# Kernel tuning notes

Measured on AMD Instinct MI355X. Metric: run time of the kernel, lower is better.

Reference implementation:

```python
import jax, jax.numpy as jnp
import numpy as np

HID = 1024
NH = 16
HD = HID // NH  # 64
RANK = 16
B, L = 2, 2048


def setup_inputs() -> dict:
    key = jax.random.key(0)
    ks = jax.random.split(key, 9)
    s = 0.02
    return {
        "x": jax.random.normal(ks[0], (B, L, HID), dtype=jnp.float32),
        "Wq": jax.random.normal(ks[1], (HID, HID), dtype=jnp.float32) * s,
        "Wk": jax.random.normal(ks[2], (HID, HID), dtype=jnp.float32) * s,
        "Wv": jax.random.normal(ks[3], (HID, HID), dtype=jnp.float32) * s,
        "Wg": jax.random.normal(ks[4], (HID, HID), dtype=jnp.float32) * s,
        "Wgk1": jax.random.normal(ks[5], (HID, RANK), dtype=jnp.float32) * s,
        "Wgk2": jax.random.normal(ks[6], (RANK, HID), dtype=jnp.float32) * s,
        "bgk2": jnp.zeros((HID,), dtype=jnp.float32),
        "gamma": jnp.ones((HID,), dtype=jnp.float32),
        "beta": jnp.zeros((HID,), dtype=jnp.float32),
        "Wout": jax.random.normal(ks[7], (HID, HID), dtype=jnp.float32) * s,
    }


def reference(x, Wq, Wk, Wv, Wg, Wgk1, Wgk2, bgk2, gamma, beta, Wout):
    Bb, Ll, Hid = x.shape
    H, Dh = NH, HD
    # projections -> [B, L, H, Dh]
    q = (x @ Wq).reshape(Bb, Ll, H, Dh)
    k = (x @ Wk).reshape(Bb, Ll, H, Dh)
    v = (x @ Wv).reshape(Bb, Ll, H, Dh)
    gk = (jax.nn.log_sigmoid((x @ Wgk1) @ Wgk2 + bgk2) / 16.0).reshape(Bb, Ll, H, Dh)

    # time-major for scan: [L, B, H, Dh]
    qT = jnp.transpose(q, (1, 0, 2, 3))
    kT = jnp.transpose(k, (1, 0, 2, 3))
    vT = jnp.transpose(v, (1, 0, 2, 3))
    gT = jnp.transpose(gk, (1, 0, 2, 3))

    def step(state, inp):
        qt, kt, vt, gt = inp  # each [B, H, Dh]
        gate = jnp.exp(gt)
        # state[b,h,v_dim,k_dim]; gate applied along v_dim (matches torch code)
        state = state * gate[..., None] + vt[..., None] * kt[..., None, :]
        out_t = jnp.einsum('bhvk,bhk->bhv', state, qt)
        return state, out_t

    state0 = jnp.zeros((Bb, H, Dh, Dh), dtype=x.dtype)
    _, outs = jax.lax.scan(step, state0, (qT, kT, vT, gT))  # outs: [L, B, H, Dh]
    out = jnp.transpose(outs, (1, 0, 2, 3)).reshape(Bb, Ll, Hid)

    # LayerNorm over total_dim
    mu = out.mean(-1, keepdims=True)
    var = out.var(-1, keepdims=True)
    out = (out - mu) / jnp.sqrt(var + 1e-5) * gamma + beta

    # output gate + projection (dropout = identity in eval)
    out = out * jax.nn.silu(x @ Wg)
    return out @ Wout
```

## Files before the change

kernel.cpp:

```cpp
#include <hip/hip_runtime.h>
#include <cstdint>
#include <cstddef>

#define HIDS 1024
#define NHEAD 16
#define HDIM 64
#define LSEQ 2048
#define BBATCH 2
#define NROW (BBATCH * LSEQ)
#define CHUNK 64
#define NCHUNK (LSEQ / CHUNK)
#define RANK 16

typedef short short8 __attribute__((ext_vector_type(8)));
typedef float floatx4 __attribute__((ext_vector_type(4)));

__device__ __forceinline__ ushort f2bf(float f) {
  uint32_t u = __float_as_uint(f);
  uint32_t r = (u + 0x7fffu + ((u >> 16) & 1u)) >> 16;
  return (ushort)r;
}
__device__ __forceinline__ float bf2f(ushort u) {
  return __uint_as_float(((uint32_t)u) << 16);
}
__device__ __forceinline__ float logsig16(float z) {
  return (fminf(z, 0.f) - log1pf(expf(-fabsf(z)))) * (1.f / 16.f);
}

__device__ __forceinline__ void async_copy16(const void* g, void* l) {
  __builtin_amdgcn_global_load_lds(
      (const __attribute__((address_space(1))) void*)g,
      (__attribute__((address_space(3))) void*)l, 16, 0, 0);
}

__global__ __launch_bounds__(256) void cvt_x_kernel(const float* __restrict__ x,
                                                    ushort* __restrict__ xbf) {
  const int i = blockIdx.x * 256 + threadIdx.x;
  float4 f = *(const float4*)(x + (size_t)i * 4);
  ushort4 o;
  o.x = f2bf(f.x); o.y = f2bf(f.y); o.z = f2bf(f.z); o.w = f2bf(f.w);
  *(ushort4*)(xbf + (size_t)i * 4) = o;
}

__global__ __launch_bounds__(256) void transpose_w_kernel(
    const float* __restrict__ W0, const float* __restrict__ W1,
    const float* __restrict__ W2, const float* __restrict__ W3,
    const float* __restrict__ W4, ushort* __restrict__ T0,
    ushort* __restrict__ T1, ushort* __restrict__ T2, ushort* __restrict__ T3,
    ushort* __restrict__ T4) {
  const int z = blockIdx.z;
  const float* W = (z == 0) ? W0 : (z == 1) ? W1 : (z == 2) ? W2 : (z == 3) ? W3 : W4;
  ushort* T = (z == 0) ? T0 : (z == 1) ? T1 : (z == 2) ? T2 : (z == 3) ? T3 : T4;
  __shared__ float sl[64][65];
  const int tid = threadIdx.x;
  const int k0 = blockIdx.y * 64, n0 = blockIdx.x * 64;
  const int r = tid >> 2, c4 = (tid & 3) * 16;
#pragma unroll
  for (int i = 0; i < 4; ++i) {
    float4 f = *(const float4*)(W + (size_t)(k0 + r) * HIDS + n0 + c4 + i * 4);
    sl[r][c4 + i * 4 + 0] = f.x;
    sl[r][c4 + i * 4 + 1] = f.y;
    sl[r][c4 + i * 4 + 2] = f.z;
    sl[r][c4 + i * 4 + 3] = f.w;
  }
  __syncthreads();
  const int n = tid >> 2, kc = (tid & 3) * 16;
#pragma unroll
  for (int i = 0; i < 4; ++i) {
    int kk = kc + i * 4;
    ushort4 o;
    o.x = f2bf(sl[kk + 0][n]);
    o.y = f2bf(sl[kk + 1][n]);
    o.z = f2bf(sl[kk + 2][n]);
    o.w = f2bf(sl[kk + 3][n]);
    *(ushort4*)(T + (size_t)(n0 + n) * HIDS + k0 + kk) = o;
  }
}

__global__ __launch_bounds__(256) void weff_kernel(const float* __restrict__ Wgk1,
                                                   const float* __restrict__ Wgk2,
                                                   ushort* __restrict__ Wte) {
  __shared__ float sW1[64][17];
  __shared__ float sW2[16][65];
  const int tid = threadIdx.x;
  const int n0 = blockIdx.x * 64, k0 = blockIdx.y * 64;
  {
    const int kl = tid >> 2, r4 = (tid & 3) * 4;
    float4 f = *(const float4*)(Wgk1 + (size_t)(k0 + kl) * RANK + r4);
    sW1[kl][r4] = f.x; sW1[kl][r4 + 1] = f.y; sW1[kl][r4 + 2] = f.z; sW1[kl][r4 + 3] = f.w;
    const int rr = tid >> 4, nl = (tid & 15) * 4;
    float4 g = *(const float4*)(Wgk2 + (size_t)rr * HIDS + n0 + nl);
    sW2[rr][nl] = g.x; sW2[rr][nl + 1] = g.y; sW2[rr][nl + 2] = g.z; sW2[rr][nl + 3] = g.w;
  }
  __syncthreads();
  const int nl = tid & 63, kq = (tid >> 6) * 16;
  float w2[16];
#pragma unroll
  for (int r = 0; r < 16; ++r) w2[r] = sW2[r][nl];
  ushort ob[16];
#pragma unroll
  for (int i = 0; i < 16; ++i) {
    float s = 0.f;
#pragma unroll
    for (int r = 0; r < 16; ++r) s = fmaf(sW1[kq + i][r], w2[r], s);
    ob[i] = f2bf(s);
  }
#pragma unroll
  for (int i = 0; i < 2; ++i)
    *(short8*)(Wte + (size_t)(n0 + nl) * HIDS + k0 + kq + i * 8) = *(short8*)&ob[i * 8];
}

__global__ __launch_bounds__(256) void proj5_kernel(
    const ushort* __restrict__ xbf, const ushort* __restrict__ Wtq,
    const ushort* __restrict__ Wtk, const ushort* __restrict__ Wtv,
    const ushort* __restrict__ Wtg, const ushort* __restrict__ Wte,
    ushort* __restrict__ qb, ushort* __restrict__ kb, ushort* __restrict__ vb,
    ushort* __restrict__ gb, ushort* __restrict__ zb) {
  const int z = blockIdx.z;
  const ushort* Bt = (z == 0) ? Wtq : (z == 1) ? Wtk : (z == 2) ? Wtv
                     : (z == 3) ? Wtg : Wte;
  ushort* C = (z == 0) ? qb : (z == 1) ? kb : (z == 2) ? vb : (z == 3) ? gb : zb;
  __shared__ ushort As[2][128 * 32];
  __shared__ ushort Bs[2][128 * 32];
  const int tid = threadIdx.x;
  const int wave = tid >> 6, lane = tid & 63;
  const int wm = (wave >> 1) * 64, wn = (wave & 1) * 64;
  const int bm = blockIdx.y * 128, bn = blockIdx.x * 128;
  const int lrow = tid >> 2, lk8 = (tid & 3) * 8;
  const ushort* Ag = xbf + (size_t)(bm + lrow) * HIDS + lk8;
  const ushort* Bg = Bt + (size_t)(bn + lrow) * HIDS + lk8;
  char* A0 = (char*)&As[0][0] + tid * 16;
  char* A1 = (char*)&As[1][0] + tid * 16;
  char* B0 = (char*)&Bs[0][0] + tid * 16;
  char* B1 = (char*)&Bs[1][0] + tid * 16;

  floatx4 acc[4][4];
#pragma unroll
  for (int i = 0; i < 4; ++i)
#pragma unroll
    for (int j = 0; j < 4; ++j) acc[i][j] = (floatx4){0.f, 0.f, 0.f, 0.f};

  const int fm = lane & 15, quad = lane >> 4;

  for (int k0 = 0; k0 < HIDS; k0 += 64) {
    __syncthreads();
    async_copy16(Ag + k0, A0);
    async_copy16(Ag + (size_t)64 * HIDS + k0, A0 + 4096);
    async_copy16(Ag + k0 + 32, A1);
    async_copy16(Ag + (size_t)64 * HIDS + k0 + 32, A1 + 4096);
    async_copy16(Bg + k0, B0);
    async_copy16(Bg + (size_t)64 * HIDS + k0, B0 + 4096);
    async_copy16(Bg + k0 + 32, B1);
    async_copy16(Bg + (size_t)64 * HIDS + k0 + 32, B1 + 4096);
    __syncthreads();

#pragma unroll
    for (int ks = 0; ks < 2; ++ks) {
      short8 af[4], bfr[4];
#pragma unroll
      for (int i = 0; i < 4; ++i)
        af[i] = *(const short8*)&As[ks][(wm + i * 16 + fm) * 32 + quad * 8];
#pragma unroll
      for (int j = 0; j < 4; ++j)
        bfr[j] = *(const short8*)&Bs[ks][(wn + j * 16 + fm) * 32 + quad * 8];
#pragma unroll
      for (int i = 0; i < 4; ++i)
#pragma unroll
        for (int j = 0; j < 4; ++j)
          acc[i][j] = __builtin_amdgcn_mfma_f32_16x16x32_bf16(af[i], bfr[j],
                                                              acc[i][j], 0, 0, 0);
    }
  }

#pragma unroll
  for (int i = 0; i < 4; ++i) {
    const int row0 = bm + wm + i * 16 + quad * 4;
#pragma unroll
    for (int j = 0; j < 4; ++j) {
      const int col = bn + wn + j * 16 + fm;
#pragma unroll
      for (int r = 0; r < 4; ++r)
        C[(size_t)(row0 + r) * HIDS + col] = f2bf(acc[i][j][r]);
    }
  }
}

__global__ __launch_bounds__(256) void gemm_out_kernel(
    const ushort* __restrict__ A, const ushort* __restrict__ Bt,
    float* __restrict__ C) {
  __shared__ ushort As[2][128 * 32];
  __shared__ ushort Bs[2][64 * 32];
  const int tid = threadIdx.x;
  const int wave = tid >> 6, lane = tid & 63;
  const int fm = lane & 15, quad = lane >> 4;
  const int bm = blockIdx.y * 128, bn = blockIdx.x * 64;
  const int lrow = tid >> 2, lk8 = (tid & 3) * 8;
  const ushort* Ag = A + (size_t)(bm + lrow) * HIDS + lk8;
  const ushort* Bg = Bt + (size_t)(bn + lrow) * HIDS + lk8;
  char* A0 = (char*)&As[0][0] + tid * 16;
  char* A1 = (char*)&As[1][0] + tid * 16;
  char* B0 = (char*)&Bs[0][0] + tid * 16;
  char* B1 = (char*)&Bs[1][0] + tid * 16;

  floatx4 acc[2][4];
#pragma unroll
  for (int i = 0; i < 2; ++i)
#pragma unroll
    for (int j = 0; j < 4; ++j) acc[i][j] = (floatx4){0.f, 0.f, 0.f, 0.f};

  for (int k0 = 0; k0 < HIDS; k0 += 64) {
    __syncthreads();
    async_copy16(Ag + k0, A0);
    async_copy16(Ag + (size_t)64 * HIDS + k0, A0 + 4096);
    async_copy16(Ag + k0 + 32, A1);
    async_copy16(Ag + (size_t)64 * HIDS + k0 + 32, A1 + 4096);
    async_copy16(Bg + k0, B0);
    async_copy16(Bg + k0 + 32, B1);
    __syncthreads();

#pragma unroll
    for (int ks = 0; ks < 2; ++ks) {
      short8 af[2], bfr[4];
#pragma unroll
      for (int i = 0; i < 2; ++i)
        af[i] = *(const short8*)&As[ks][(wave * 32 + i * 16 + fm) * 32 + quad * 8];
#pragma unroll
      for (int j = 0; j < 4; ++j)
        bfr[j] = *(const short8*)&Bs[ks][(j * 16 + fm) * 32 + quad * 8];
#pragma unroll
      for (int i = 0; i < 2; ++i)
#pragma unroll
        for (int j = 0; j < 4; ++j)
          acc[i][j] = __builtin_amdgcn_mfma_f32_16x16x32_bf16(af[i], bfr[j],
                                                              acc[i][j], 0, 0, 0);
    }
  }

#pragma unroll
  for (int i = 0; i < 2; ++i) {
    const int row0 = bm + wave * 32 + i * 16 + quad * 4;
#pragma unroll
    for (int j = 0; j < 4; ++j) {
      const int col = bn + j * 16 + fm;
#pragma unroll
      for (int r = 0; r < 4; ++r)
        C[(size_t)(row0 + r) * HIDS + col] = acc[i][j][r];
    }
  }
}

#define SP 72
#define SGS 68

__global__ __launch_bounds__(256) void sdelta_kernel(
    const ushort* __restrict__ k, const ushort* __restrict__ v,
    const ushort* __restrict__ zb, const float* __restrict__ bgk2,
    ushort* __restrict__ Sdelta, float* __restrict__ Lam) {
  const int bid = blockIdx.x;
  const int c = bid & 31, bh = bid >> 5;
  const int b = bh >> 4, h = bh & 15;
  const int tid = threadIdx.x;
  const int lane = tid & 63, wave = tid >> 6;
  const int fm = lane & 15, quad = lane >> 4;
  const int wm2 = (wave >> 1) * 32, wn2 = (wave & 1) * 32;

  __shared__ ushort sKt[64 * SP];
  __shared__ ushort sVt[64 * SP];
  __shared__ float sG[64 * SGS];

  const size_t base = ((size_t)b * LSEQ + (size_t)c * CHUNK) * HIDS + (size_t)h * HDIM;
  const int r = tid >> 2, c0 = (tid & 3) * 16;
  const size_t gb = base + (size_t)r * HIDS + c0;
  {
    float bias[16];
#pragma unroll
    for (int m = 0; m < 4; ++m)
      *(float4*)&bias[m * 4] = *(const float4*)(bgk2 + h * HDIM + c0 + m * 4);
    short8 z0 = *(const short8*)(zb + gb);
    short8 z1 = *(const short8*)(zb + gb + 8);
#pragma unroll
    for (int i = 0; i < 16; ++i) {
      float zz = bf2f((ushort)(i < 8 ? z0[i] : z1[i - 8])) + bias[i];
      sG[r * SGS + c0 + i] = logsig16(zz);
    }
  }
  const int pr = (tid >> 3) * 2, pc = (tid & 7) * 8;
  const size_t pb = base + (size_t)pr * HIDS + pc;
  short8 ka = *(const short8*)(k + pb);
  short8 kb2 = *(const short8*)(k + pb + HIDS);
  short8 va = *(const short8*)(v + pb);
  short8 vb2 = *(const short8*)(v + pb + HIDS);
  __syncthreads();

  const int vcol = tid & 63, qtr = tid >> 6;
  {
    float run = 0.f;
#pragma unroll
    for (int i = 0; i < 16; ++i) {
      int idx = (qtr * 16 + i) * SGS + vcol;
      run += sG[idx];
      sG[idx] = run;
    }
  }
  __syncthreads();
  float pre = 0.f;
  for (int j = 0; j < qtr; ++j) pre += sG[(j * 16 + 15) * SGS + vcol];
  __syncthreads();
#pragma unroll
  for (int i = 0; i < 16; ++i) sG[(qtr * 16 + i) * SGS + vcol] += pre;
  __syncthreads();

#pragma unroll
  for (int i = 0; i < 8; ++i) {
    ushort2 kk;
    kk.x = (ushort)ka[i];
    kk.y = (ushort)kb2[i];
    *(ushort2*)&sKt[(pc + i) * SP + pr] = kk;
    float Ga = sG[pr * SGS + pc + i];
    float Gb2 = sG[(pr + 1) * SGS + pc + i];
    ushort2 vv;
    vv.x = f2bf(bf2f((ushort)va[i]) * expf(-Ga));
    vv.y = f2bf(bf2f((ushort)vb2[i]) * expf(-Gb2));
    *(ushort2*)&sVt[(pc + i) * SP + pr] = vv;
  }
  __syncthreads();

  if (tid < 64)
    Lam[(size_t)(bh * NCHUNK + c) * HDIM + tid] = expf(sG[63 * SGS + tid]);

  floatx4 accD[2][2];
#pragma unroll
  for (int i = 0; i < 2; ++i)
#pragma unroll
    for (int j = 0; j < 2; ++j) accD[i][j] = (floatx4){0.f, 0.f, 0.f, 0.f};
#pragma unroll
  for (int ks = 0; ks < 2; ++ks) {
    short8 av[2], bk[2];
#pragma unroll
    for (int i = 0; i < 2; ++i)
      av[i] = *(const short8*)&sVt[(wm2 + i * 16 + fm) * SP + ks * 32 + quad * 8];
#pragma unroll
    for (int j = 0; j < 2; ++j)
      bk[j] = *(const short8*)&sKt[(wn2 + j * 16 + fm) * SP + ks * 32 + quad * 8];
#pragma unroll
    for (int i = 0; i < 2; ++i)
#pragma unroll
      for (int j = 0; j < 2; ++j)
        accD[i][j] = __builtin_amdgcn_mfma_f32_16x16x32_bf16(av[i], bk[j],
                                                             accD[i][j], 0, 0, 0);
  }
  const size_t sbase = (size_t)(bh * NCHUNK + c) * (HDIM * HDIM);
#pragma unroll
  for (int i = 0; i < 2; ++i) {
    const int m0 = wm2 + i * 16 + quad * 4;
    float lam[4];
#pragma unroll
    for (int rr = 0; rr < 4; ++rr) lam[rr] = expf(sG[63 * SGS + m0 + rr]);
#pragma unroll
    for (int j = 0; j < 2; ++j) {
      const int n = wn2 + j * 16 + fm;
#pragma unroll
      for (int rr = 0; rr < 4; ++rr)
        Sdelta[sbase + (size_t)(m0 + rr) * HDIM + n] = f2bf(accD[i][j][rr] * lam[rr]);
    }
  }
}

__global__ __launch_bounds__(256) void state_scan_kernel(
    const ushort* __restrict__ Sdelta, const float* __restrict__ Lam,
    ushort* __restrict__ Sprev) {
  const int bh = blockIdx.x;
  const int tid = threadIdx.x;
  float S[16];
#pragma unroll
  for (int i = 0; i < 16; ++i) S[i] = 0.f;

  float pd[16], pl[16];
  {
    const size_t base = (size_t)(bh * NCHUNK) * (HDIM * HDIM);
    const size_t lbase = (size_t)(bh * NCHUNK) * HDIM;
#pragma unroll
    for (int i = 0; i < 16; ++i) {
      int e = tid + 256 * i;
      pd[i] = bf2f(Sdelta[base + e]);
      pl[i] = Lam[lbase + (e >> 6)];
    }
  }
  for (int c = 0; c < NCHUNK; ++c) {
    float cd[16], cl[16];
#pragma unroll
    for (int i = 0; i < 16; ++i) { cd[i] = pd[i]; cl[i] = pl[i]; }
    if (c + 1 < NCHUNK) {
      const size_t base = (size_t)(bh * NCHUNK + c + 1) * (HDIM * HDIM);
      const size_t lbase = (size_t)(bh * NCHUNK + c + 1) * HDIM;
#pragma unroll
      for (int i = 0; i < 16; ++i) {
        int e = tid + 256 * i;
        pd[i] = bf2f(Sdelta[base + e]);
        pl[i] = Lam[lbase + (e >> 6)];
      }
    }
    const size_t obase = (size_t)(bh * NCHUNK + c) * (HDIM * HDIM);
#pragma unroll
    for (int i = 0; i < 16; ++i) {
      int e = tid + 256 * i;
      Sprev[obase + e] = f2bf(S[i]);
      S[i] = fmaf(S[i], cl[i], cd[i]);
    }
  }
}

__global__ __launch_bounds__(256) void chunk_fused_kernel(
    const ushort* __restrict__ q, const ushort* __restrict__ k,
    const ushort* __restrict__ v, const ushort* __restrict__ zb,
    const float* __restrict__ bgk2, const ushort* __restrict__ Sprev,
    ushort* __restrict__ att) {
  const int bid = blockIdx.x;
  const int c = bid & 31, bh = bid >> 5;
  const int b = bh >> 4, h = bh & 15;
  const int tid = threadIdx.x;
  const int lane = tid & 63, wave = tid >> 6;
  const int fm = lane & 15, quad = lane >> 4;
  const int wm2 = (wave >> 1) * 32, wn2 = (wave & 1) * 32;

  __shared__ ushort sQ[64 * SP];
  __shared__ ushort sK[64 * SP];
  __shared__ ushort sVt[64 * SP];
  __shared__ ushort sSp[64 * SP];
  __shared__ ushort sA[64 * SP];
  __shared__ float sG[64 * SGS];

  const size_t base = ((size_t)b * LSEQ + (size_t)c * CHUNK) * HIDS + (size_t)h * HDIM;
  const size_t sbase = (size_t)(bh * NCHUNK + c) * (HDIM * HDIM);
  const int r = tid >> 2, c0 = (tid & 3) * 16;
  const size_t gb = base + (size_t)r * HIDS + c0;
  *(short8*)&sQ[r * SP + c0] = *(const short8*)(q + gb);
  *(short8*)&sQ[r * SP + c0 + 8] = *(const short8*)(q + gb + 8);
  *(short8*)&sK[r * SP + c0] = *(const short8*)(k + gb);
  *(short8*)&sK[r * SP + c0 + 8] = *(const short8*)(k + gb + 8);
  {
    float bias[16];
#pragma unroll
    for (int m = 0; m < 4; ++m)
      *(float4*)&bias[m * 4] = *(const float4*)(bgk2 + h * HDIM + c0 + m * 4);
    short8 z0 = *(const short8*)(zb + gb);
    short8 z1 = *(const short8*)(zb + gb + 8);
#pragma unroll
    for (int i = 0; i < 16; ++i) {
      float zz = bf2f((ushort)(i < 8 ? z0[i] : z1[i - 8])) + bias[i];
      sG[r * SGS + c0 + i] = logsig16(zz);
    }
  }
  *(short8*)&sSp[r * SP + c0] = *(const short8*)(Sprev + sbase + (size_t)r * HDIM + c0);
  *(short8*)&sSp[r * SP + c0 + 8] =
      *(const short8*)(Sprev + sbase + (size_t)r * HDIM + c0 + 8);
  const int pr = (tid >> 3) * 2, pc = (tid & 7) * 8;
  const size_t pb = base + (size_t)pr * HIDS + pc;
  short8 va = *(const short8*)(v + pb);
  short8 vb2 = *(const short8*)(v + pb + HIDS);
  __syncthreads();

  const int vcol = tid & 63, qtr = tid >> 6;
  {
    float run = 0.f;
#pragma unroll
    for (int i = 0; i < 16; ++i) {
      int idx = (qtr * 16 + i) * SGS + vcol;
      run += sG[idx];
      sG[idx] = run;
    }
  }
  __syncthreads();
  float pre = 0.f;
  for (int j = 0; j < qtr; ++j) pre += sG[(j * 16 + 15) * SGS + vcol];
  __syncthreads();
#pragma unroll
  for (int i = 0; i < 16; ++i) sG[(qtr * 16 + i) * SGS + vcol] += pre;
  __syncthreads();

#pragma unroll
  for (int i = 0; i < 8; ++i) {
    float Ga = sG[pr * SGS + pc + i];
    float Gb2 = sG[(pr + 1) * SGS + pc + i];
    ushort2 vv;
    vv.x = f2bf(bf2f((ushort)va[i]) * expf(-Ga));
    vv.y = f2bf(bf2f((ushort)vb2[i]) * expf(-Gb2));
    *(ushort2*)&sVt[(pc + i) * SP + pr] = vv;
  }
  __syncthreads();

  {
    floatx4 acc[2][2];
#pragma unroll
    for (int i = 0; i < 2; ++i)
#pragma unroll
      for (int j = 0; j < 2; ++j) acc[i][j] = (floatx4){0.f, 0.f, 0.f, 0.f};
#pragma unroll
    for (int ks = 0; ks < 2; ++ks) {
      short8 a[2], bb[2];
#pragma unroll
      for (int i = 0; i < 2; ++i)
        a[i] = *(const short8*)&sQ[(wm2 + i * 16 + fm) * SP + ks * 32 + quad * 8];
#pragma unroll
      for (int j = 0; j < 2; ++j)
        bb[j] = *(const short8*)&sK[(wn2 + j * 16 + fm) * SP + ks * 32 + quad * 8];
#pragma unroll
      for (int i = 0; i < 2; ++i)
#pragma unroll
        for (int j = 0; j < 2; ++j)
          acc[i][j] = __builtin_amdgcn_mfma_f32_16x16x32_bf16(a[i], bb[j],
                                                              acc[i][j], 0, 0, 0);
    }
#pragma unroll
    for (int i = 0; i < 2; ++i)
#pragma unroll
      for (int j = 0; j < 2; ++j) {
        const int t0 = wm2 + i * 16 + quad * 4;
        const int s = wn2 + j * 16 + fm;
#pragma unroll
        for (int rr = 0; rr < 4; ++rr) {
          float val = (s <= t0 + rr) ? acc[i][j][rr] : 0.f;
          sA[(t0 + rr) * SP + s] = f2bf(val);
        }
      }
  }
  __syncthreads();

  floatx4 acc[2][2];
#pragma unroll
  for (int i = 0; i < 2; ++i)
#pragma unroll
    for (int j = 0; j < 2; ++j) acc[i][j] = (floatx4){0.f, 0.f, 0.f, 0.f};
#pragma unroll
  for (int ks = 0; ks < 2; ++ks) {
    short8 aa[2], aq[2], bv[2], bs[2];
#pragma unroll
    for (int i = 0; i < 2; ++i) {
      aa[i] = *(const short8*)&sA[(wm2 + i * 16 + fm) * SP + ks * 32 + quad * 8];
      aq[i] = *(const short8*)&sQ[(wm2 + i * 16 + fm) * SP + ks * 32 + quad * 8];
    }
#pragma unroll
    for (int j = 0; j < 2; ++j) {
      bv[j] = *(const short8*)&sVt[(wn2 + j * 16 + fm) * SP + ks * 32 + quad * 8];
      bs[j] = *(const short8*)&sSp[(wn2 + j * 16 + fm) * SP + ks * 32 + quad * 8];
    }
#pragma unroll
    for (int i = 0; i < 2; ++i)
#pragma unroll
      for (int j = 0; j < 2; ++j) {
        acc[i][j] = __builtin_amdgcn_mfma_f32_16x16x32_bf16(aa[i], bv[j],
                                                            acc[i][j], 0, 0, 0);
        acc[i][j] = __builtin_amdgcn_mfma_f32_16x16x32_bf16(aq[i], bs[j],
                                                            acc[i][j], 0, 0, 0);
      }
  }
#pragma unroll
  for (int i = 0; i < 2; ++i)
#pragma unroll
    for (int j = 0; j < 2; ++j) {
      const int m0 = wm2 + i * 16 + quad * 4;
      const int n = wn2 + j * 16 + fm;
#pragma unroll
      for (int rr = 0; rr < 4; ++rr) {
        const int m = m0 + rr;
        att[base + (size_t)m * HIDS + n] =
            f2bf(acc[i][j][rr] * expf(sG[m * SGS + n]));
      }
    }
}

__global__ __launch_bounds__(256) void ln_gate_kernel(const ushort* __restrict__ att,
                                                      const ushort* __restrict__ g,
                                                      const float* __restrict__ gamma,
                                                      const float* __restrict__ beta,
                                                      ushort* __restrict__ ybf) {
  const int row = blockIdx.x;
  const int tid = threadIdx.x;
  ushort4 au = *(const ushort4*)(att + (size_t)row * HIDS + tid * 4);
  float ax = bf2f(au.x), ay = bf2f(au.y), az = bf2f(au.z), aw = bf2f(au.w);
  float s = ax + ay + az + aw;
  float ss = ax * ax + ay * ay + az * az + aw * aw;
#pragma unroll
  for (int off = 32; off; off >>= 1) {
    s += __shfl_down(s, off);
    ss += __shfl_down(ss, off);
  }
  __shared__ float rs[4], rss[4];
  const int wid = tid >> 6;
  if ((tid & 63) == 0) { rs[wid] = s; rss[wid] = ss; }
  __syncthreads();
  const float mean = (rs[0] + rs[1] + rs[2] + rs[3]) * (1.f / HIDS);
  const float ex2 = (rss[0] + rss[1] + rss[2] + rss[3]) * (1.f / HIDS);
  const float rstd = rsqrtf(ex2 - mean * mean + 1e-5f);

  float4 ga = *(const float4*)(gamma + tid * 4);
  float4 be = *(const float4*)(beta + tid * 4);
  ushort4 gu = *(const ushort4*)(g + (size_t)row * HIDS + tid * 4);
  float gx = bf2f(gu.x), gy = bf2f(gu.y), gz = bf2f(gu.z), gw = bf2f(gu.w);
  float4 o;
  o.x = ((ax - mean) * rstd * ga.x + be.x) * (gx / (1.f + expf(-gx)));
  o.y = ((ay - mean) * rstd * ga.y + be.y) * (gy / (1.f + expf(-gy)));
  o.z = ((az - mean) * rstd * ga.z + be.z) * (gz / (1.f + expf(-gz)));
  o.w = ((aw - mean) * rstd * ga.w + be.w) * (gw / (1.f + expf(-gw)));
  ushort4 ob;
  ob.x = f2bf(o.x); ob.y = f2bf(o.y); ob.z = f2bf(o.z); ob.w = f2bf(o.w);
  *(ushort4*)(ybf + (size_t)row * HIDS + tid * 4) = ob;
}

extern "C" void kernel_launch(void* const* d_in, const int* in_sizes, int n_in,
                              void* d_out, int out_size, void* d_ws, size_t ws_size,
                              hipStream_t stream) {
  const float* x     = (const float*)d_in[0];
  const float* Wq    = (const float*)d_in[1];
  const float* Wk    = (const float*)d_in[2];
  const float* Wv    = (const float*)d_in[3];
  const float* Wg    = (const float*)d_in[4];
  const float* Wgk1  = (const float*)d_in[5];
  const float* Wgk2  = (const float*)d_in[6];
  const float* bgk2  = (const float*)d_in[7];
  const float* gamma = (const float*)d_in[8];
  const float* beta  = (const float*)d_in[9];
  const float* Wout  = (const float*)d_in[10];
  float* out = (float*)d_out;

  const size_t SZ = (size_t)NROW * HIDS;
  float* ws = (float*)d_ws;
  float* Lamb = ws;
  ushort* attb   = (ushort*)(ws + 65536);
  ushort* Sdelta = attb + SZ;
  ushort* Sprevb = Sdelta + SZ;
  ushort* qbf = Sprevb + SZ;
  ushort* kbf = qbf + SZ;
  ushort* vbf = kbf + SZ;
  ushort* gbf = vbf + SZ;
  ushort* zbf = gbf + SZ;
  ushort* xbf = zbf + SZ;
  ushort* Wtq = xbf + SZ;
  ushort* Wtk = Wtq + HIDS * HIDS;
  ushort* Wtv = Wtk + HIDS * HIDS;
  ushort* Wtg = Wtv + HIDS * HIDS;
  ushort* Wto = Wtg + HIDS * HIDS;
  ushort* Wte = Wto + HIDS * HIDS;
  ushort* ybf = vbf;

  cvt_x_kernel<<<SZ / 1024, 256, 0, stream>>>(x, xbf);
  transpose_w_kernel<<<dim3(16, 16, 5), 256, 0, stream>>>(
      Wq, Wk, Wv, Wg, Wout, Wtq, Wtk, Wtv, Wtg, Wto);
  weff_kernel<<<dim3(16, 16), 256, 0, stream>>>(Wgk1, Wgk2, Wte);

  proj5_kernel<<<dim3(HIDS / 128, NROW / 128, 5), 256, 0, stream>>>(
      xbf, Wtq, Wtk, Wtv, Wtg, Wte, qbf, kbf, vbf, gbf, zbf);

  sdelta_kernel<<<BBATCH * NHEAD * NCHUNK, 256, 0, stream>>>(
      kbf, vbf, zbf, bgk2, Sdelta, Lamb);
  state_scan_kernel<<<BBATCH * NHEAD, 256, 0, stream>>>(Sdelta, Lamb, Sprevb);
  chunk_fused_kernel<<<BBATCH * NHEAD * NCHUNK, 256, 0, stream>>>(
      qbf, kbf, vbf, zbf, bgk2, Sprevb, attb);

  ln_gate_kernel<<<NROW, 256, 0, stream>>>(attb, gbf, gamma, beta, ybf);
  gemm_out_kernel<<<dim3(HIDS / 64, NROW / 128), 256, 0, stream>>>(ybf, Wto, out);
}
```

Before: 240.4 us.

## Merge prep kernels, widen state scan grid, alias Sprev into K shared buffer

Folds the three weight and input preparation kernels into one launch that dispatches on block index, which removes launch gaps. The inter-chunk state scan is split across 8 blocks per batch-head (256 blocks instead of 32), so each thread carries two state elements instead of sixteen and more of the GPU is used. The chunk kernel now reuses the K shared buffer for the previous state, with an extra barrier, to cut LDS use and raise occupancy. The Sprev load is issued early into registers so its latency overlaps the other loads.

```diff
diff --git a/kernel.cpp b/kernel.cpp
--- a/kernel.cpp
+++ b/kernel.cpp
@@ -33,81 +33,86 @@
       (__attribute__((address_space(3))) void*)l, 16, 0, 0);
 }
 
-__global__ __launch_bounds__(256) void cvt_x_kernel(const float* __restrict__ x,
-                                                    ushort* __restrict__ xbf) {
-  const int i = blockIdx.x * 256 + threadIdx.x;
-  float4 f = *(const float4*)(x + (size_t)i * 4);
-  ushort4 o;
-  o.x = f2bf(f.x); o.y = f2bf(f.y); o.z = f2bf(f.z); o.w = f2bf(f.w);
-  *(ushort4*)(xbf + (size_t)i * 4) = o;
-}
-
-__global__ __launch_bounds__(256) void transpose_w_kernel(
+__global__ __launch_bounds__(256) void prep_kernel(
+    const float* __restrict__ x, ushort* __restrict__ xbf,
     const float* __restrict__ W0, const float* __restrict__ W1,
     const float* __restrict__ W2, const float* __restrict__ W3,
     const float* __restrict__ W4, ushort* __restrict__ T0,
     ushort* __restrict__ T1, ushort* __restrict__ T2, ushort* __restrict__ T3,
-    ushort* __restrict__ T4) {
-  const int z = blockIdx.z;
-  const float* W = (z == 0) ? W0 : (z == 1) ? W1 : (z == 2) ? W2 : (z == 3) ? W3 : W4;
-  ushort* T = (z == 0) ? T0 : (z == 1) ? T1 : (z == 2) ? T2 : (z == 3) ? T3 : T4;
-  __shared__ float sl[64][65];
+    ushort* __restrict__ T4, const float* __restrict__ Wgk1,
+    const float* __restrict__ Wgk2, ushort* __restrict__ Wte) {
+  __shared__ float sbuf[64 * 65];
+  const int bid = blockIdx.x;
   const int tid = threadIdx.x;
-  const int k0 = blockIdx.y * 64, n0 = blockIdx.x * 64;
-  const int r = tid >> 2, c4 = (tid & 3) * 16;
-#pragma unroll
-  for (int i = 0; i < 4; ++i) {
-    float4 f = *(const float4*)(W + (size_t)(k0 + r) * HIDS + n0 + c4 + i * 4);
-    sl[r][c4 + i * 4 + 0] = f.x;
-    sl[r][c4 + i * 4 + 1] = f.y;
-    sl[r][c4 + i * 4 + 2] = f.z;
-    sl[r][c4 + i * 4 + 3] = f.w;
-  }
-  __syncthreads();
-  const int n = tid >> 2, kc = (tid & 3) * 16;
-#pragma unroll
-  for (int i = 0; i < 4; ++i) {
-    int kk = kc + i * 4;
+
+  if (bid < 4096) {
+    const int i = bid * 256 + tid;
+    float4 f = *(const float4*)(x + (size_t)i * 4);
     ushort4 o;
-    o.x = f2bf(sl[kk + 0][n]);
-    o.y = f2bf(sl[kk + 1][n]);
-    o.z = f2bf(sl[kk + 2][n]);
-    o.w = f2bf(sl[kk + 3][n]);
-    *(ushort4*)(T + (size_t)(n0 + n) * HIDS + k0 + kk) = o;
-  }
-}
-
-__global__ __launch_bounds__(256) void weff_kernel(const float* __restrict__ Wgk1,
-                                                   const float* __restrict__ Wgk2,
-                                                   ushort* __restrict__ Wte) {
-  __shared__ float sW1[64][17];
-  __shared__ float sW2[16][65];
-  const int tid = threadIdx.x;
-  const int n0 = blockIdx.x * 64, k0 = blockIdx.y * 64;
-  {
-    const int kl = tid >> 2, r4 = (tid & 3) * 4;
-    float4 f = *(const float4*)(Wgk1 + (size_t)(k0 + kl) * RANK + r4);
-    sW1[kl][r4] = f.x; sW1[kl][r4 + 1] = f.y; sW1[kl][r4 + 2] = f.z; sW1[kl][r4 + 3] = f.w;
-    const int rr = tid >> 4, nl = (tid & 15) * 4;
-    float4 g = *(const float4*)(Wgk2 + (size_t)rr * HIDS + n0 + nl);
-    sW2[rr][nl] = g.x; sW2[rr][nl + 1] = g.y; sW2[rr][nl + 2] = g.z; sW2[rr][nl + 3] = g.w;
-  }
-  __syncthreads();
-  const int nl = tid & 63, kq = (tid >> 6) * 16;
-  float w2[16];
-#pragma unroll
-  for (int r = 0; r < 16; ++r) w2[r] = sW2[r][nl];
-  ushort ob[16];
-#pragma unroll
-  for (int i = 0; i < 16; ++i) {
-    float s = 0.f;
-#pragma unroll
-    for (int r = 0; r < 16; ++r) s = fmaf(sW1[kq + i][r], w2[r], s);
-    ob[i] = f2bf(s);
-  }
-#pragma unroll
-  for (int i = 0; i < 2; ++i)
-    *(short8*)(Wte + (size_t)(n0 + nl) * HIDS + k0 + kq + i * 8) = *(short8*)&ob[i * 8];
+    o.x = f2bf(f.x); o.y = f2bf(f.y); o.z = f2bf(f.z); o.w = f2bf(f.w);
+    *(ushort4*)(xbf + (size_t)i * 4) = o;
+  } else if (bid < 5376) {
+    const int w = bid - 4096;
+    const int z = w >> 8, rem = w & 255;
+    const float* W = (z == 0) ? W0 : (z == 1) ? W1 : (z == 2) ? W2
+                     : (z == 3) ? W3 : W4;
+    ushort* T = (z == 0) ? T0 : (z == 1) ? T1 : (z == 2) ? T2
+                : (z == 3) ? T3 : T4;
+    const int k0 = (rem >> 4) * 64, n0 = (rem & 15) * 64;
+    const int r = tid >> 2, c4 = (tid & 3) * 16;
+#pragma unroll
+    for (int i = 0; i < 4; ++i) {
+      float4 f = *(const float4*)(W + (size_t)(k0 + r) * HIDS + n0 + c4 + i * 4);
+      sbuf[r * 65 + c4 + i * 4 + 0] = f.x;
+      sbuf[r * 65 + c4 + i * 4 + 1] = f.y;
+      sbuf[r * 65 + c4 + i * 4 + 2] = f.z;
+      sbuf[r * 65 + c4 + i * 4 + 3] = f.w;
+    }
+    __syncthreads();
+    const int n = tid >> 2, kc = (tid & 3) * 16;
+#pragma unroll
+    for (int i = 0; i < 4; ++i) {
+      int kk = kc + i * 4;
+      ushort4 o;
+      o.x = f2bf(sbuf[(kk + 0) * 65 + n]);
+      o.y = f2bf(sbuf[(kk + 1) * 65 + n]);
+      o.z = f2bf(sbuf[(kk + 2) * 65 + n]);
+      o.w = f2bf(sbuf[(kk + 3) * 65 + n]);
+      *(ushort4*)(T + (size_t)(n0 + n) * HIDS + k0 + kk) = o;
+    }
+  } else {
+    const int rem = bid - 5376;
+    const int n0 = (rem & 15) * 64, k0 = (rem >> 4) * 64;
+    float* sW1 = sbuf;
+    float* sW2 = sbuf + 64 * 17;
+    {
+      const int kl = tid >> 2, r4 = (tid & 3) * 4;
+      float4 f = *(const float4*)(Wgk1 + (size_t)(k0 + kl) * RANK + r4);
+      sW1[kl * 17 + r4] = f.x; sW1[kl * 17 + r4 + 1] = f.y;
+      sW1[kl * 17 + r4 + 2] = f.z; sW1[kl * 17 + r4 + 3] = f.w;
+      const int rr = tid >> 4, nl = (tid & 15) * 4;
+      float4 g = *(const float4*)(Wgk2 + (size_t)rr * HIDS + n0 + nl);
+      sW2[rr * 65 + nl] = g.x; sW2[rr * 65 + nl + 1] = g.y;
+      sW2[rr * 65 + nl + 2] = g.z; sW2[rr * 65 + nl + 3] = g.w;
+    }
+    __syncthreads();
+    const int nl = tid & 63, kq = (tid >> 6) * 16;
+    float w2[16];
+#pragma unroll
+    for (int r = 0; r < 16; ++r) w2[r] = sW2[r * 65 + nl];
+    ushort ob[16];
+#pragma unroll
+    for (int i = 0; i < 16; ++i) {
+      float s = 0.f;
+#pragma unroll
+      for (int r = 0; r < 16; ++r) s = fmaf(sW1[(kq + i) * 17 + r], w2[r], s);
+      ob[i] = f2bf(s);
+    }
+#pragma unroll
+    for (int i = 0; i < 2; ++i)
+      *(short8*)(Wte + (size_t)(n0 + nl) * HIDS + k0 + kq + i * 8) =
+          *(short8*)&ob[i * 8];
+  }
 }
 
 __global__ __launch_bounds__(256) void proj5_kernel(
@@ -369,44 +374,34 @@
 __global__ __launch_bounds__(256) void state_scan_kernel(
     const ushort* __restrict__ Sdelta, const float* __restrict__ Lam,
     ushort* __restrict__ Sprev) {
-  const int bh = blockIdx.x;
+  const int bh = blockIdx.x >> 3;
+  const int sl = blockIdx.x & 7;
   const int tid = threadIdx.x;
-  float S[16];
-#pragma unroll
-  for (int i = 0; i < 16; ++i) S[i] = 0.f;
-
-  float pd[16], pl[16];
-  {
-    const size_t base = (size_t)(bh * NCHUNK) * (HDIM * HDIM);
-    const size_t lbase = (size_t)(bh * NCHUNK) * HDIM;
-#pragma unroll
-    for (int i = 0; i < 16; ++i) {
-      int e = tid + 256 * i;
-      pd[i] = bf2f(Sdelta[base + e]);
-      pl[i] = Lam[lbase + (e >> 6)];
-    }
-  }
+  const int e0 = sl * 512 + tid;
+  float S0 = 0.f, S1 = 0.f;
+
+  size_t base = (size_t)(bh * NCHUNK) * (HDIM * HDIM);
+  size_t lbase = (size_t)(bh * NCHUNK) * HDIM;
+  float pd0 = bf2f(Sdelta[base + e0]);
+  float pd1 = bf2f(Sdelta[base + e0 + 256]);
+  float pl0 = Lam[lbase + (e0 >> 6)];
+  float pl1 = Lam[lbase + ((e0 + 256) >> 6)];
+
   for (int c = 0; c < NCHUNK; ++c) {
-    float cd[16], cl[16];
-#pragma unroll
-    for (int i = 0; i < 16; ++i) { cd[i] = pd[i]; cl[i] = pl[i]; }
+    float cd0 = pd0, cd1 = pd1, cl0 = pl0, cl1 = pl1;
     if (c + 1 < NCHUNK) {
-      const size_t base = (size_t)(bh * NCHUNK + c + 1) * (HDIM * HDIM);
-      const size_t lbase = (size_t)(bh * NCHUNK + c + 1) * HDIM;
-#pragma unroll
-      for (int i = 0; i < 16; ++i) {
-        int e = tid + 256 * i;
-        pd[i] = bf2f(Sdelta[base + e]);
-        pl[i] = Lam[lbase + (e >> 6)];
-      }
-    }
-    const size_t obase = (size_t)(bh * NCHUNK + c) * (HDIM * HDIM);
-#pragma unroll
-    for (int i = 0; i < 16; ++i) {
-      int e = tid + 256 * i;
-      Sprev[obase + e] = f2bf(S[i]);
-      S[i] = fmaf(S[i], cl[i], cd[i]);
-    }
+      size_t nb = (size_t)(bh * NCHUNK + c + 1) * (HDIM * HDIM);
+      size_t nl = (size_t)(bh * NCHUNK + c + 1) * HDIM;
+      pd0 = bf2f(Sdelta[nb + e0]);
+      pd1 = bf2f(Sdelta[nb + e0 + 256]);
+      pl0 = Lam[nl + (e0 >> 6)];
+      pl1 = Lam[nl + ((e0 + 256) >> 6)];
+    }
+    size_t ob = (size_t)(bh * NCHUNK + c) * (HDIM * HDIM);
+    Sprev[ob + e0] = f2bf(S0);
+    Sprev[ob + e0 + 256] = f2bf(S1);
+    S0 = fmaf(S0, cl0, cd0);
+    S1 = fmaf(S1, cl1, cd1);
   }
 }
 
@@ -426,14 +421,16 @@
   __shared__ ushort sQ[64 * SP];
   __shared__ ushort sK[64 * SP];
   __shared__ ushort sVt[64 * SP];
-  __shared__ ushort sSp[64 * SP];
   __shared__ ushort sA[64 * SP];
   __shared__ float sG[64 * SGS];
+  ushort* sSp = sK;
 
   const size_t base = ((size_t)b * LSEQ + (size_t)c * CHUNK) * HIDS + (size_t)h * HDIM;
   const size_t sbase = (size_t)(bh * NCHUNK + c) * (HDIM * HDIM);
   const int r = tid >> 2, c0 = (tid & 3) * 16;
   const size_t gb = base + (size_t)r * HIDS + c0;
+  short8 sp0 = *(const short8*)(Sprev + sbase + (size_t)r * HDIM + c0);
+  short8 sp1 = *(const short8*)(Sprev + sbase + (size_t)r * HDIM + c0 + 8);
   *(short8*)&sQ[r * SP + c0] = *(const short8*)(q + gb);
   *(short8*)&sQ[r * SP + c0 + 8] = *(const short8*)(q + gb + 8);
   *(short8*)&sK[r * SP + c0] = *(const short8*)(k + gb);
@@ -451,9 +448,6 @@
       sG[r * SGS + c0 + i] = logsig16(zz);
     }
   }
-  *(short8*)&sSp[r * SP + c0] = *(const short8*)(Sprev + sbase + (size_t)r * HDIM + c0);
-  *(short8*)&sSp[r * SP + c0 + 8] =
-      *(const short8*)(Sprev + sbase + (size_t)r * HDIM + c0 + 8);
   const int pr = (tid >> 3) * 2, pc = (tid & 7) * 8;
   const size_t pb = base + (size_t)pr * HIDS + pc;
   short8 va = *(const short8*)(v + pb);
@@ -489,41 +483,43 @@
   }
   __syncthreads();
 
-  {
-    floatx4 acc[2][2];
+  floatx4 accS[2][2];
+#pragma unroll
+  for (int i = 0; i < 2; ++i)
+#pragma unroll
+    for (int j = 0; j < 2; ++j) accS[i][j] = (floatx4){0.f, 0.f, 0.f, 0.f};
+#pragma unroll
+  for (int ks = 0; ks < 2; ++ks) {
+    short8 a[2], bb[2];
 #pragma unroll
     for (int i = 0; i < 2; ++i)
-#pragma unroll
-      for (int j = 0; j < 2; ++j) acc[i][j] = (floatx4){0.f, 0.f, 0.f, 0.f};
-#pragma unroll
-    for (int ks = 0; ks < 2; ++ks) {
-      short8 a[2], bb[2];
-#pragma unroll
-      for (int i = 0; i < 2; ++i)
-        a[i] = *(const short8*)&sQ[(wm2 + i * 16 + fm) * SP + ks * 32 + quad * 8];
+      a[i] = *(const short8*)&sQ[(wm2 + i * 16 + fm) * SP + ks * 32 + quad * 8];
+#pragma unroll
+    for (int j = 0; j < 2; ++j)
+      bb[j] = *(const short8*)&sK[(wn2 + j * 16 + fm) * SP + ks * 32 + quad * 8];
+#pragma unroll
+    for (int i = 0; i < 2; ++i)
 #pragma unroll
       for (int j = 0; j < 2; ++j)
-        bb[j] = *(const short8*)&sK[(wn2 + j * 16 + fm) * SP + ks * 32 + quad * 8];
-#pragma unroll
-      for (int i = 0; i < 2; ++i)
-#pragma unroll
-        for (int j = 0; j < 2; ++j)
-          acc[i][j] = __builtin_amdgcn_mfma_f32_16x16x32_bf16(a[i], bb[j],
-                                                              acc[i][j], 0, 0, 0);
-    }
-#pragma unroll
-    for (int i = 0; i < 2; ++i)
-#pragma unroll
-      for (int j = 0; j < 2; ++j) {
-        const int t0 = wm2 + i * 16 + quad * 4;
-        const int s = wn2 + j * 16 + fm;
-#pragma unroll
-        for (int rr = 0; rr < 4; ++rr) {
-          float val = (s <= t0 + rr) ? acc[i][j][rr] : 0.f;
-          sA[(t0 + rr) * SP + s] = f2bf(val);
-        }
+        accS[i][j] = __builtin_amdgcn_mfma_f32_16x16x32_bf16(a[i], bb[j],
+                                                             accS[i][j], 0, 0, 0);
+  }
+  __syncthreads();
+
+#pragma unroll
+  for (int i = 0; i < 2; ++i)
+#pragma unroll
+    for (int j = 0; j < 2; ++j) {
+      const int t0 = wm2 + i * 16 + quad * 4;
+      const int s = wn2 + j * 16 + fm;
+#pragma unroll
+      for (int rr = 0; rr < 4; ++rr) {
+        float val = (s <= t0 + rr) ? accS[i][j][rr] : 0.f;
+        sA[(t0 + rr) * SP + s] = f2bf(val);
       }
-  }
+    }
+  *(short8*)&sSp[r * SP + c0] = sp0;
+  *(short8*)&sSp[r * SP + c0 + 8] = sp1;
   __syncthreads();
 
   floatx4 acc[2][2];
@@ -643,17 +639,15 @@
   ushort* Wte = Wto + HIDS * HIDS;
   ushort* ybf = vbf;
 
-  cvt_x_kernel<<<SZ / 1024, 256, 0, stream>>>(x, xbf);
-  transpose_w_kernel<<<dim3(16, 16, 5), 256, 0, stream>>>(
-      Wq, Wk, Wv, Wg, Wout, Wtq, Wtk, Wtv, Wtg, Wto);
-  weff_kernel<<<dim3(16, 16), 256, 0, stream>>>(Wgk1, Wgk2, Wte);
+  prep_kernel<<<4096 + 1280 + 256, 256, 0, stream>>>(
+      x, xbf, Wq, Wk, Wv, Wg, Wout, Wtq, Wtk, Wtv, Wtg, Wto, Wgk1, Wgk2, Wte);
 
   proj5_kernel<<<dim3(HIDS / 128, NROW / 128, 5), 256, 0, stream>>>(
       xbf, Wtq, Wtk, Wtv, Wtg, Wte, qbf, kbf, vbf, gbf, zbf);
 
   sdelta_kernel<<<BBATCH * NHEAD * NCHUNK, 256, 0, stream>>>(
       kbf, vbf, zbf, bgk2, Sdelta, Lamb);
-  state_scan_kernel<<<BBATCH * NHEAD, 256, 0, stream>>>(Sdelta, Lamb, Sprevb);
+  state_scan_kernel<<<256, 256, 0, stream>>>(Sdelta, Lamb, Sprevb);
   chunk_fused_kernel<<<BBATCH * NHEAD * NCHUNK, 256, 0, stream>>>(
       qbf, kbf, vbf, zbf, bgk2, Sprevb, attb);
 
```

Result: faster. 224.7 us (-6.5%).
